# Optimization experiments

Hardware: AMD Instinct MI355X
Metric: run time of the kernel (lower is better)

The kernel has to match this reference:

```python
import jax, jax.numpy as jnp
import numpy as np

DIM = 256
NUM_HEADS = 4
HEAD_DIM = DIM // NUM_HEADS
SCALE = HEAD_DIM ** -0.5


def setup_inputs() -> dict:
    key = jax.random.key(0)
    ks = jax.random.split(key, 9)
    B, P, C = 4, 4096, DIM
    s = 0.02
    return {
        "x": jax.random.normal(ks[0], (B, P, C), dtype=jnp.float32),
        "Wq": jax.random.normal(ks[1], (C, C), dtype=jnp.float32) * s,
        "bq": jnp.zeros((C,), dtype=jnp.float32),
        "Wk": jax.random.normal(ks[2], (C, C), dtype=jnp.float32) * s,
        "bk": jnp.zeros((C,), dtype=jnp.float32),
        "Wv": jax.random.normal(ks[3], (C, C), dtype=jnp.float32) * s,
        "bv": jnp.zeros((C,), dtype=jnp.float32),
        "Wo": jax.random.normal(ks[4], (C, C), dtype=jnp.float32) * s,
        "bo": jnp.zeros((C,), dtype=jnp.float32),
    }


def reference(x, Wq, bq, Wk, bk, Wv, bv, Wo, bo):
    B, P, C = x.shape
    H, D = NUM_HEADS, C // NUM_HEADS
    q = (x @ Wq + bq).reshape(B, P, H, D)
    k = (x @ Wk + bk).reshape(B, P, H, D)
    v = (x @ Wv + bv).reshape(B, P, H, D)
    # att[b,p,q,h] = sum_d q[b,p,h,d]*scale * k[b,q,h,d]
    att = jnp.einsum('bphd,bqhd->bpqh', q * SCALE, k)
    att = jax.nn.softmax(att, axis=2)
    out = jnp.einsum('bpqh,bqhd->bphd', att, v).reshape(B, P, C)
    return out @ Wo + bo
```

## Files before the change

### kernel.cpp

```cpp
#include <hip/hip_runtime.h>
#include <hip/hip_bf16.h>

#define DIMC 256
#define NHEADS 4
#define HDIM 64
#define BATCH 4
#define SEQ 4096
#define MTOT (BATCH*SEQ)
#define SCALE_LOG2E 0.18033688011112042f

typedef __attribute__((ext_vector_type(8))) __bf16 bf16x8;
typedef __attribute__((ext_vector_type(4))) __bf16 bf16x4;
typedef __attribute__((ext_vector_type(2))) __bf16 bf16x2;
typedef __attribute__((ext_vector_type(4))) float f32x4;
typedef __attribute__((ext_vector_type(16))) float f32x16;
typedef __attribute__((ext_vector_type(2))) unsigned uint2v;
typedef __attribute__((ext_vector_type(4))) unsigned uint4v;

__device__ inline void gll16(const void* g, void* l) {
  __builtin_amdgcn_global_load_lds((const __attribute__((address_space(1))) unsigned int*)g,
                                   (__attribute__((address_space(3))) unsigned int*)l, 16, 0, 0);
}

__device__ inline float vexp2(float x) { return __builtin_amdgcn_exp2f(x); }

__device__ inline unsigned pack2(float lo, float hi) {
  bf16x2 p; p[0] = (__bf16)lo; p[1] = (__bf16)hi;
  return __builtin_bit_cast(unsigned, p);
}

__device__ inline bf16x8 swzread(const __bf16* base, int row, int c16) {
  return *reinterpret_cast<const bf16x8*>(
      reinterpret_cast<const char*>(base) + row * 128 + ((c16 ^ (row & 7)) << 4));
}


__global__ __launch_bounds__(256) void cvt_x_kernel(const float* __restrict__ x, __bf16* __restrict__ xb) {
  int i = (blockIdx.x * 256 + threadIdx.x) * 4;
  float4 v = *reinterpret_cast<const float4*>(x + i);
  bf16x4 o;
  o[0] = (__bf16)v.x; o[1] = (__bf16)v.y; o[2] = (__bf16)v.z; o[3] = (__bf16)v.w;
  *reinterpret_cast<bf16x4*>(xb + i) = o;
}

__global__ __launch_bounds__(256) void prep_w(const float* __restrict__ Wq, const float* __restrict__ Wk,
                                              const float* __restrict__ Wv, const float* __restrict__ Wo,
                                              const float* __restrict__ bq, const float* __restrict__ bk,
                                              const float* __restrict__ bv,
                                              __bf16* __restrict__ wqkvt, __bf16* __restrict__ wot,
                                              float* __restrict__ biasq) {
  int row = blockIdx.x;
  int k = threadIdx.x;
  if (row < 768) {
    const float* src; float scale = 1.f; int n = row & 255;
    if (row < 256)      { src = Wq; scale = SCALE_LOG2E; }
    else if (row < 512) { src = Wk; }
    else                { src = Wv; }
    wqkvt[row * 256 + k] = (__bf16)(src[k * 256 + n] * scale);
  } else if (row < 1024) {
    int n = row - 768;
    wot[n * 256 + k] = (__bf16)(Wo[k * 256 + n]);
  } else {
    int i = (row - 1024) * 256 + k;
    biasq[i] = (i < 256) ? bq[i] * SCALE_LOG2E : (i < 512 ? bk[i - 256] : bv[i - 512]);
  }
}

template<int MODE>
__global__ __launch_bounds__(256) void gemm_bt(const __bf16* __restrict__ A, const __bf16* __restrict__ Bt,
                                               const float* __restrict__ bias,
                                               __bf16* __restrict__ q_ws, __bf16* __restrict__ k_ws,
                                               __bf16* __restrict__ vt_ws, float* __restrict__ fout) {
  __shared__ __align__(16) __bf16 As[128 * 64];
  __shared__ __align__(16) __bf16 Bs[128 * 64];
  const int tid = threadIdx.x;
  const int lane = tid & 63, wave = tid >> 6;
  const int wr = wave >> 1, wc = wave & 1;
  const int r16 = lane & 15, g4 = lane >> 4;
  const int m0 = blockIdx.y * 128, n0 = blockIdx.x * 128;
  f32x4 acc[4][4] = {};
  for (int k0 = 0; k0 < DIMC; k0 += 64) {
    #pragma unroll
    for (int it = 0; it < 4; ++it) {
      int e = it * 256 + tid;
      int r = e >> 3, c = e & 7;
      int cs = c ^ (r & 7);
      gll16(A  + (size_t)(m0 + r) * DIMC + k0 + cs * 8, As + e * 8);
      gll16(Bt + (size_t)(n0 + r) * DIMC + k0 + cs * 8, Bs + e * 8);
    }
    __syncthreads();
    #pragma unroll
    for (int kk = 0; kk < 2; ++kk) {
      bf16x8 af[4], bfr[4];
      #pragma unroll
      for (int mi = 0; mi < 4; ++mi)
        af[mi] = swzread(As, wr * 64 + mi * 16 + r16, kk * 4 + g4);
      #pragma unroll
      for (int ni = 0; ni < 4; ++ni)
        bfr[ni] = swzread(Bs, wc * 64 + ni * 16 + r16, kk * 4 + g4);
      #pragma unroll
      for (int mi = 0; mi < 4; ++mi)
        #pragma unroll
        for (int ni = 0; ni < 4; ++ni)
          acc[mi][ni] = __builtin_amdgcn_mfma_f32_16x16x32_bf16(af[mi], bfr[ni], acc[mi][ni], 0, 0, 0);
    }
    __syncthreads();
  }
  #pragma unroll
  for (int mi = 0; mi < 4; ++mi)
    #pragma unroll
    for (int ni = 0; ni < 4; ++ni)
      #pragma unroll
      for (int r = 0; r < 4; ++r) {
        int m = m0 + wr * 64 + mi * 16 + g4 * 4 + r;
        int n = n0 + wc * 64 + ni * 16 + r16;
        float v = acc[mi][ni][r] + bias[n];
        if (MODE == 0) {
          int b = m >> 12, p = m & 4095;
          int sect = n >> 8, nc = n & 255;
          int h = nc >> 6, d = nc & 63;
          __bf16 hv = (__bf16)v;
          size_t bhb = (size_t)(b * NHEADS + h);
          if (sect == 0)      q_ws[(bhb * SEQ + p) * HDIM + d] = hv;
          else if (sect == 1) k_ws[(bhb * SEQ + p) * HDIM + d] = hv;
          else                vt_ws[(bhb * HDIM + d) * SEQ + p] = hv;
        } else {
          fout[(size_t)m * DIMC + n] = v;
        }
      }
}

__global__ __launch_bounds__(256, 4) void attn_kernel(const __bf16* __restrict__ q_ws, const __bf16* __restrict__ k_ws,
                                                      const __bf16* __restrict__ vt_ws,
                                                      __bf16* __restrict__ o_part, float* __restrict__ lsum_part) {
  __shared__ __align__(16) __bf16 Ks[2][64 * 64];
  __shared__ __align__(16) __bf16 Vts[2][64 * 64];
  const int tid = threadIdx.x;
  const int lane = tid & 63;
  const int l31 = lane & 31, h5 = lane >> 5;
  int bid = blockIdx.x;
  int wg = (bid & 7) * 128 + (bid >> 3);
  int bh = wg >> 6, rrw = wg & 63;
  int qb = rrw >> 1, half = rrw & 1;
  int b = bh >> 2, h = bh & 3;
  const __bf16* Qp  = q_ws  + (size_t)bh * SEQ * HDIM;
  const __bf16* Kp  = k_ws  + (size_t)bh * SEQ * HDIM;
  const __bf16* Vtp = vt_ws + (size_t)bh * HDIM * SEQ;
  const int q0 = qb * 128 + (tid >> 6) * 32;
  const int kvb = half * (SEQ / 2);
  bf16x8 qf[4];
  #pragma unroll
  for (int ks = 0; ks < 4; ++ks)
    qf[ks] = *reinterpret_cast<const bf16x8*>(Qp + (size_t)(q0 + l31) * HDIM + ks * 16 + h5 * 8);
  f32x16 o_acc[2] = {};
  f32x4 dv = {};

  const int sr = tid >> 3;
  const int scs = (tid & 7) ^ (sr & 7);
  const __bf16* kSrc = Kp  + (size_t)sr * HDIM + scs * 8;
  const __bf16* vSrc = Vtp + (size_t)sr * SEQ  + scs * 8;

  #define STAGE(buf, kv0) do { \
      gll16(kSrc + (size_t)(kv0) * HDIM,        &Ks[buf][tid * 8]); \
      gll16(kSrc + (size_t)((kv0) + 32) * HDIM, &Ks[buf][(tid + 256) * 8]); \
      gll16(vSrc + (kv0),                       &Vts[buf][tid * 8]); \
      gll16(vSrc + 32 * SEQ + (kv0),            &Vts[buf][(tid + 256) * 8]); \
    } while (0)

  #define TILE(BUF, DO_STAGE, kv0_next) do { \
    if (DO_STAGE) STAGE(BUF ^ 1, kv0_next); \
    f32x16 s[2] = {}; \
    __builtin_amdgcn_s_setprio(1); \
    _Pragma("unroll") \
    for (int ni = 0; ni < 2; ++ni) \
      _Pragma("unroll") \
      for (int ks = 0; ks < 4; ++ks) { \
        bf16x8 kf = swzread(Ks[BUF], ni * 32 + l31, ks * 2 + h5); \
        s[ni] = __builtin_amdgcn_mfma_f32_32x32x16_bf16(kf, qf[ks], s[ni], 0, 0, 0); \
      } \
    __builtin_amdgcn_s_setprio(0); \
    float E[2][16]; \
    _Pragma("unroll") \
    for (int ni = 0; ni < 2; ++ni) \
      _Pragma("unroll") \
      for (int r = 0; r < 16; ++r) { \
        float e = vexp2(s[ni][r]); \
        E[ni][r] = e; \
        dv[r & 3] += e; \
      } \
    bf16x8 pa[4]; \
    _Pragma("unroll") \
    for (int ks = 0; ks < 4; ++ks) { \
      const int ni = ks >> 1, base = (ks & 1) * 8; \
      unsigned A0 = pack2(E[ni][base + 0], E[ni][base + 1]); \
      unsigned A1 = pack2(E[ni][base + 2], E[ni][base + 3]); \
      unsigned B0 = pack2(E[ni][base + 4], E[ni][base + 5]); \
      unsigned B1 = pack2(E[ni][base + 6], E[ni][base + 7]); \
      uint2v r0 = __builtin_amdgcn_permlane32_swap(A0, B0, false, false); \
      uint2v r1 = __builtin_amdgcn_permlane32_swap(A1, B1, false, false); \
      uint4v wv = {r0[0], r1[0], r0[1], r1[1]}; \
      pa[ks] = __builtin_bit_cast(bf16x8, wv); \
    } \
    __builtin_amdgcn_s_setprio(1); \
    _Pragma("unroll") \
    for (int ks = 0; ks < 4; ++ks) \
      _Pragma("unroll") \
      for (int di = 0; di < 2; ++di) { \
        bf16x8 vf = swzread(Vts[BUF], di * 32 + l31, ks * 2 + h5); \
        o_acc[di] = __builtin_amdgcn_mfma_f32_32x32x16_bf16(pa[ks], vf, o_acc[di], 0, 0, 0); \
      } \
    __builtin_amdgcn_s_setprio(0); \
    __syncthreads(); \
  } while (0)

  STAGE(0, kvb);
  __syncthreads();

  const int NT = SEQ / 128;
  for (int tt = 0; tt < NT; tt += 2) {
    TILE(0, true,           kvb + (tt + 1) * 64);
    TILE(1, (tt + 2) < NT,  kvb + (tt + 2) * 64);
  }

  float den = (dv[0] + dv[1]) + (dv[2] + dv[3]);
  den += __shfl_xor(den, 32);
  if (lane < 32) lsum_part[(size_t)half * 16 * SEQ + (size_t)bh * SEQ + q0 + l31] = den;
  __bf16* op = o_part + (size_t)half * MTOT * DIMC;
  #pragma unroll
  for (int di = 0; di < 2; ++di)
    #pragma unroll
    for (int r = 0; r < 16; ++r) {
      int q = q0 + (r & 3) + 8 * (r >> 2) + 4 * h5;
      op[(size_t)(b * SEQ + q) * DIMC + h * HDIM + di * 32 + l31] = (__bf16)o_acc[di][r];
    }
}

__global__ __launch_bounds__(256) void combine_o(const __bf16* __restrict__ o_part,
                                                 const float* __restrict__ lsum_part,
                                                 __bf16* __restrict__ o_ws) {
  int i = blockIdx.x * 256 + threadIdx.x;
  int flat = i * 8;
  int m = flat >> 8, c = flat & 255;
  int h = c >> 6;
  int b = m >> 12, p = m & 4095;
  size_t bhp = (size_t)(b * NHEADS + h) * SEQ + p;
  float inv = 1.f / (lsum_part[bhp] + lsum_part[(size_t)16 * SEQ + bhp]);
  bf16x8 a = *reinterpret_cast<const bf16x8*>(o_part + flat);
  bf16x8 bb = *reinterpret_cast<const bf16x8*>(o_part + (size_t)MTOT * DIMC + flat);
  bf16x8 o;
  #pragma unroll
  for (int j = 0; j < 8; ++j)
    o[j] = (__bf16)(((float)a[j] + (float)bb[j]) * inv);
  *reinterpret_cast<bf16x8*>(o_ws + flat) = o;
}


extern "C" void kernel_launch(void* const* d_in, const int* in_sizes, int n_in,
                              void* d_out, int out_size, void* d_ws, size_t ws_size,
                              hipStream_t stream) {
  const float* x  = (const float*)d_in[0];
  const float* Wq = (const float*)d_in[1];
  const float* bq = (const float*)d_in[2];
  const float* Wk = (const float*)d_in[3];
  const float* bk = (const float*)d_in[4];
  const float* Wv = (const float*)d_in[5];
  const float* bv = (const float*)d_in[6];
  const float* Wo = (const float*)d_in[7];
  const float* bo = (const float*)d_in[8];
  float* out = (float*)d_out;

  const size_t NE = (size_t)MTOT * DIMC;
  char* w = (char*)d_ws;
  __bf16* q_ws   = (__bf16*)w; w += NE * 2;
  __bf16* k_ws   = (__bf16*)w; w += NE * 2;
  __bf16* vt_ws  = (__bf16*)w; w += NE * 2;
  __bf16* wqkvt  = (__bf16*)w; w += (size_t)768 * 256 * 2;
  __bf16* wot    = (__bf16*)w; w += (size_t)256 * 256 * 2;
  float*  biasq  = (float*)w;  w += 768 * 4;
  float*  lsum_p = (float*)w;  w += (size_t)2 * 16 * SEQ * 4;
  __bf16* o_part = (__bf16*)w; w += 2 * NE * 2;
  __bf16* xb   = o_part;
  __bf16* o_ws = q_ws;

  cvt_x_kernel<<<MTOT * DIMC / 1024, 256, 0, stream>>>(x, xb);
  prep_w<<<1027, 256, 0, stream>>>(Wq, Wk, Wv, Wo, bq, bk, bv, wqkvt, wot, biasq);
  gemm_bt<0><<<dim3(6, 128), 256, 0, stream>>>(xb, wqkvt, biasq, q_ws, k_ws, vt_ws, nullptr);
  attn_kernel<<<1024, 256, 0, stream>>>(q_ws, k_ws, vt_ws, o_part, lsum_p);
  combine_o<<<NE / 2048, 256, 0, stream>>>(o_part, lsum_p, o_ws);
  gemm_bt<1><<<dim3(2, 128), 256, 0, stream>>>(o_ws, wot, bo, nullptr, nullptr, nullptr, out);
}
```

Baseline: 128.7 us.

## Give each attention wave 64 queries and split keys into quarters

```diff
diff --git a/kernel.cpp b/kernel.cpp
--- a/kernel.cpp
+++ b/kernel.cpp
@@ -130,9 +130,10 @@
       }
 }
 
-__global__ __launch_bounds__(256, 4) void attn_kernel(const __bf16* __restrict__ q_ws, const __bf16* __restrict__ k_ws,
+__global__ __launch_bounds__(256, 3) void attn_kernel(const __bf16* __restrict__ q_ws, const __bf16* __restrict__ k_ws,
                                                       const __bf16* __restrict__ vt_ws,
-                                                      __bf16* __restrict__ o_part, float* __restrict__ lsum_part) {
+                                                      __bf16* __restrict__ o01, __bf16* __restrict__ o23,
+                                                      float* __restrict__ lsum_part) {
   __shared__ __align__(16) __bf16 Ks[2][64 * 64];
   __shared__ __align__(16) __bf16 Vts[2][64 * 64];
   const int tid = threadIdx.x;
@@ -140,20 +141,22 @@
   const int l31 = lane & 31, h5 = lane >> 5;
   int bid = blockIdx.x;
   int wg = (bid & 7) * 128 + (bid >> 3);
-  int bh = wg >> 6, rrw = wg & 63;
-  int qb = rrw >> 1, half = rrw & 1;
+  int bh = wg >> 6, sub = wg & 63;
+  int qb = sub >> 2, quarter = sub & 3;
   int b = bh >> 2, h = bh & 3;
   const __bf16* Qp  = q_ws  + (size_t)bh * SEQ * HDIM;
   const __bf16* Kp  = k_ws  + (size_t)bh * SEQ * HDIM;
   const __bf16* Vtp = vt_ws + (size_t)bh * HDIM * SEQ;
-  const int q0 = qb * 128 + (tid >> 6) * 32;
-  const int kvb = half * (SEQ / 2);
-  bf16x8 qf[4];
-  #pragma unroll
-  for (int ks = 0; ks < 4; ++ks)
-    qf[ks] = *reinterpret_cast<const bf16x8*>(Qp + (size_t)(q0 + l31) * HDIM + ks * 16 + h5 * 8);
-  f32x16 o_acc[2] = {};
-  f32x4 dv = {};
+  const int q0 = qb * 256 + (tid >> 6) * 64;
+  const int kvb = quarter * (SEQ / 4);
+  bf16x8 qf[2][4];
+  #pragma unroll
+  for (int hh = 0; hh < 2; ++hh)
+    #pragma unroll
+    for (int ks = 0; ks < 4; ++ks)
+      qf[hh][ks] = *reinterpret_cast<const bf16x8*>(Qp + (size_t)(q0 + hh * 32 + l31) * HDIM + ks * 16 + h5 * 8);
+  f32x16 o_acc[2][2] = {};
+  f32x4 dv0 = {}, dv1 = {};
 
   const int sr = tid >> 3;
   const int scs = (tid & 7) ^ (sr & 7);
@@ -169,37 +172,47 @@
 
   #define TILE(BUF, DO_STAGE, kv0_next) do { \
     if (DO_STAGE) STAGE(BUF ^ 1, kv0_next); \
-    f32x16 s[2] = {}; \
-    __builtin_amdgcn_s_setprio(1); \
+    bf16x8 pa0[4], pa1[4]; \
     _Pragma("unroll") \
-    for (int ni = 0; ni < 2; ++ni) \
+    for (int ni = 0; ni < 2; ++ni) { \
+      f32x16 s0 = {}, s1 = {}; \
+      __builtin_amdgcn_s_setprio(1); \
       _Pragma("unroll") \
       for (int ks = 0; ks < 4; ++ks) { \
         bf16x8 kf = swzread(Ks[BUF], ni * 32 + l31, ks * 2 + h5); \
-        s[ni] = __builtin_amdgcn_mfma_f32_32x32x16_bf16(kf, qf[ks], s[ni], 0, 0, 0); \
+        s0 = __builtin_amdgcn_mfma_f32_32x32x16_bf16(kf, qf[0][ks], s0, 0, 0, 0); \
+        s1 = __builtin_amdgcn_mfma_f32_32x32x16_bf16(kf, qf[1][ks], s1, 0, 0, 0); \
       } \
-    __builtin_amdgcn_s_setprio(0); \
-    float E[2][16]; \
-    _Pragma("unroll") \
-    for (int ni = 0; ni < 2; ++ni) \
+      __builtin_amdgcn_s_setprio(0); \
       _Pragma("unroll") \
       for (int r = 0; r < 16; ++r) { \
-        float e = vexp2(s[ni][r]); \
-        E[ni][r] = e; \
-        dv[r & 3] += e; \
+        s0[r] = vexp2(s0[r]); dv0[r & 3] += s0[r]; \
+        s1[r] = vexp2(s1[r]); dv1[r & 3] += s1[r]; \
       } \
-    bf16x8 pa[4]; \
-    _Pragma("unroll") \
-    for (int ks = 0; ks < 4; ++ks) { \
-      const int ni = ks >> 1, base = (ks & 1) * 8; \
-      unsigned A0 = pack2(E[ni][base + 0], E[ni][base + 1]); \
-      unsigned A1 = pack2(E[ni][base + 2], E[ni][base + 3]); \
-      unsigned B0 = pack2(E[ni][base + 4], E[ni][base + 5]); \
-      unsigned B1 = pack2(E[ni][base + 6], E[ni][base + 7]); \
-      uint2v r0 = __builtin_amdgcn_permlane32_swap(A0, B0, false, false); \
-      uint2v r1 = __builtin_amdgcn_permlane32_swap(A1, B1, false, false); \
-      uint4v wv = {r0[0], r1[0], r0[1], r1[1]}; \
-      pa[ks] = __builtin_bit_cast(bf16x8, wv); \
+      _Pragma("unroll") \
+      for (int u = 0; u < 2; ++u) { \
+        const int base = u * 8, ks2 = ni * 2 + u; \
+        { \
+          unsigned A0 = pack2(s0[base + 0], s0[base + 1]); \
+          unsigned A1 = pack2(s0[base + 2], s0[base + 3]); \
+          unsigned B0 = pack2(s0[base + 4], s0[base + 5]); \
+          unsigned B1 = pack2(s0[base + 6], s0[base + 7]); \
+          uint2v r0v = __builtin_amdgcn_permlane32_swap(A0, B0, false, false); \
+          uint2v r1v = __builtin_amdgcn_permlane32_swap(A1, B1, false, false); \
+          uint4v wv = {r0v[0], r1v[0], r0v[1], r1v[1]}; \
+          pa0[ks2] = __builtin_bit_cast(bf16x8, wv); \
+        } \
+        { \
+          unsigned A0 = pack2(s1[base + 0], s1[base + 1]); \
+          unsigned A1 = pack2(s1[base + 2], s1[base + 3]); \
+          unsigned B0 = pack2(s1[base + 4], s1[base + 5]); \
+          unsigned B1 = pack2(s1[base + 6], s1[base + 7]); \
+          uint2v r0v = __builtin_amdgcn_permlane32_swap(A0, B0, false, false); \
+          uint2v r1v = __builtin_amdgcn_permlane32_swap(A1, B1, false, false); \
+          uint4v wv = {r0v[0], r1v[0], r0v[1], r1v[1]}; \
+          pa1[ks2] = __builtin_bit_cast(bf16x8, wv); \
+        } \
+      } \
     } \
     __builtin_amdgcn_s_setprio(1); \
     _Pragma("unroll") \
@@ -207,7 +220,8 @@
       _Pragma("unroll") \
       for (int di = 0; di < 2; ++di) { \
         bf16x8 vf = swzread(Vts[BUF], di * 32 + l31, ks * 2 + h5); \
-        o_acc[di] = __builtin_amdgcn_mfma_f32_32x32x16_bf16(pa[ks], vf, o_acc[di], 0, 0, 0); \
+        o_acc[0][di] = __builtin_amdgcn_mfma_f32_32x32x16_bf16(pa0[ks], vf, o_acc[0][di], 0, 0, 0); \
+        o_acc[1][di] = __builtin_amdgcn_mfma_f32_32x32x16_bf16(pa1[ks], vf, o_acc[1][di], 0, 0, 0); \
       } \
     __builtin_amdgcn_s_setprio(0); \
     __syncthreads(); \
@@ -216,26 +230,31 @@
   STAGE(0, kvb);
   __syncthreads();
 
-  const int NT = SEQ / 128;
+  const int NT = SEQ / 4 / 64;
   for (int tt = 0; tt < NT; tt += 2) {
     TILE(0, true,           kvb + (tt + 1) * 64);
     TILE(1, (tt + 2) < NT,  kvb + (tt + 2) * 64);
   }
 
-  float den = (dv[0] + dv[1]) + (dv[2] + dv[3]);
-  den += __shfl_xor(den, 32);
-  if (lane < 32) lsum_part[(size_t)half * 16 * SEQ + (size_t)bh * SEQ + q0 + l31] = den;
-  __bf16* op = o_part + (size_t)half * MTOT * DIMC;
-  #pragma unroll
-  for (int di = 0; di < 2; ++di)
-    #pragma unroll
-    for (int r = 0; r < 16; ++r) {
-      int q = q0 + (r & 3) + 8 * (r >> 2) + 4 * h5;
-      op[(size_t)(b * SEQ + q) * DIMC + h * HDIM + di * 32 + l31] = (__bf16)o_acc[di][r];
-    }
-}
-
-__global__ __launch_bounds__(256) void combine_o(const __bf16* __restrict__ o_part,
+  __bf16* op = (quarter < 2 ? o01 : o23) + (size_t)(quarter & 1) * MTOT * DIMC;
+  float* lp = lsum_part + (size_t)quarter * 16 * SEQ + (size_t)bh * SEQ;
+  #pragma unroll
+  for (int hh = 0; hh < 2; ++hh) {
+    const f32x4& dvh = hh ? dv1 : dv0;
+    float den = (dvh[0] + dvh[1]) + (dvh[2] + dvh[3]);
+    den += __shfl_xor(den, 32);
+    if (lane < 32) lp[q0 + hh * 32 + l31] = den;
+    #pragma unroll
+    for (int di = 0; di < 2; ++di)
+      #pragma unroll
+      for (int r = 0; r < 16; ++r) {
+        int q = q0 + hh * 32 + (r & 3) + 8 * (r >> 2) + 4 * h5;
+        op[(size_t)(b * SEQ + q) * DIMC + h * HDIM + di * 32 + l31] = (__bf16)o_acc[hh][di][r];
+      }
+  }
+}
+
+__global__ __launch_bounds__(256) void combine_o(const __bf16* __restrict__ o01, const __bf16* __restrict__ o23,
                                                  const float* __restrict__ lsum_part,
                                                  __bf16* __restrict__ o_ws) {
   int i = blockIdx.x * 256 + threadIdx.x;
@@ -244,13 +263,18 @@
   int h = c >> 6;
   int b = m >> 12, p = m & 4095;
   size_t bhp = (size_t)(b * NHEADS + h) * SEQ + p;
-  float inv = 1.f / (lsum_part[bhp] + lsum_part[(size_t)16 * SEQ + bhp]);
-  bf16x8 a = *reinterpret_cast<const bf16x8*>(o_part + flat);
-  bf16x8 bb = *reinterpret_cast<const bf16x8*>(o_part + (size_t)MTOT * DIMC + flat);
+  float l = 0.f;
+  #pragma unroll
+  for (int qr = 0; qr < 4; ++qr) l += lsum_part[(size_t)qr * 16 * SEQ + bhp];
+  float inv = 1.f / l;
+  bf16x8 a0 = *reinterpret_cast<const bf16x8*>(o01 + flat);
+  bf16x8 a1 = *reinterpret_cast<const bf16x8*>(o01 + (size_t)MTOT * DIMC + flat);
+  bf16x8 a2 = *reinterpret_cast<const bf16x8*>(o23 + flat);
+  bf16x8 a3 = *reinterpret_cast<const bf16x8*>(o23 + (size_t)MTOT * DIMC + flat);
   bf16x8 o;
   #pragma unroll
   for (int j = 0; j < 8; ++j)
-    o[j] = (__bf16)(((float)a[j] + (float)bb[j]) * inv);
+    o[j] = (__bf16)((((float)a0[j] + (float)a1[j]) + ((float)a2[j] + (float)a3[j])) * inv);
   *reinterpret_cast<bf16x8*>(o_ws + flat) = o;
 }
 
@@ -277,15 +301,16 @@
   __bf16* wqkvt  = (__bf16*)w; w += (size_t)768 * 256 * 2;
   __bf16* wot    = (__bf16*)w; w += (size_t)256 * 256 * 2;
   float*  biasq  = (float*)w;  w += 768 * 4;
-  float*  lsum_p = (float*)w;  w += (size_t)2 * 16 * SEQ * 4;
-  __bf16* o_part = (__bf16*)w; w += 2 * NE * 2;
-  __bf16* xb   = o_part;
+  float*  lsum_p = (float*)w;  w += (size_t)4 * 16 * SEQ * 4;
+  __bf16* o01    = (__bf16*)w; w += 2 * NE * 2;
+  __bf16* o23 = (__bf16*)out;
+  __bf16* xb   = o01;
   __bf16* o_ws = q_ws;
 
   cvt_x_kernel<<<MTOT * DIMC / 1024, 256, 0, stream>>>(x, xb);
   prep_w<<<1027, 256, 0, stream>>>(Wq, Wk, Wv, Wo, bq, bk, bv, wqkvt, wot, biasq);
   gemm_bt<0><<<dim3(6, 128), 256, 0, stream>>>(xb, wqkvt, biasq, q_ws, k_ws, vt_ws, nullptr);
-  attn_kernel<<<1024, 256, 0, stream>>>(q_ws, k_ws, vt_ws, o_part, lsum_p);
-  combine_o<<<NE / 2048, 256, 0, stream>>>(o_part, lsum_p, o_ws);
+  attn_kernel<<<1024, 256, 0, stream>>>(q_ws, k_ws, vt_ws, o01, o23, lsum_p);
+  combine_o<<<NE / 2048, 256, 0, stream>>>(o01, o23, lsum_p, o_ws);
   gemm_bt<1><<<dim3(2, 128), 256, 0, stream>>>(o_ws, wot, bo, nullptr, nullptr, nullptr, out);
 }
```

After: 279.2 us. 117% more time.
